# Kernel optimization log

Hardware: AMD Instinct MI355X
Metric: run time of the kernel (lower is better)

The kernel has to match this reference:

```python
import jax, jax.numpy as jnp
import numpy as np

H = 64          # nhid
L = 2           # nlayer
N_LEFT = 100000
N_RIGHT = 100000
E = 1000000
EPS = 1e-5

PNAMES = ["nn1_w1", "nn1_b1", "nn1_w2", "nn1_b2",
          "nn2_w1", "nn2_b1", "nn2_w2", "nn2_b2",
          "l1_w", "l1_b", "l2_w", "l2_b", "l3_w", "l3_b", "l4_w", "l4_b",
          "out_w1", "out_b1", "out_w2", "out_b2"]


def _bn_relu(x):
    # BatchNorm1d (training-mode batch stats, affine=False / default-init affine) + ReLU
    m = x.mean(0, keepdims=True)
    v = jnp.mean((x - m) ** 2, axis=0, keepdims=True)  # biased var, as torch BN
    return jax.nn.relu((x - m) * jax.lax.rsqrt(v + EPS))


def _mlp2(x, w1, b1, w2, b2):
    # MLP(nin, nout, nlayer=2, with_final_activation=True): (Linear->BN->ReLU) x2
    h = _bn_relu(x @ w1 + b1)
    return _bn_relu(h @ w2 + b2)


def _lin_bn_relu(x, w, b):
    # nn.Linear -> BatchNorm1d(affine=False) -> ReLU
    return _bn_relu(x @ w + b)


def _gscatter(msg, idx, n):
    # generalized_scatter with aggregators ['add','mean','max'], concatenated
    s = jax.ops.segment_sum(msg, idx, num_segments=n)
    cnt = jax.ops.segment_sum(jnp.ones((msg.shape[0],), msg.dtype), idx, num_segments=n)[:, None]
    mean = s / jnp.maximum(cnt, 1.0)
    mx = jax.ops.segment_max(msg, idx, num_segments=n)
    mx = jnp.where(cnt > 0, mx, 0.0)  # empty segments -> 0
    return jnp.concatenate([s, mean, mx], axis=-1)  # [n, 3*d]


def _parallel_layer(xs, src, dst, nl, p):
    # nl = n_left (static). combined_batch = [0]*nl + [1]*nr (sorted), last = 1.
    nr = xs.shape[0] - nl
    x_right = xs[nl:]                                   # batch != 0
    right_info = _gscatter(x_right[dst], src, nl)       # [nl, 3H]
    x_left_new = _mlp2(xs, p["nn1_w1"], p["nn1_b1"], p["nn1_w2"], p["nn1_b2"])[:nl]
    left_info = _gscatter(x_left_new[src], dst, nr)     # [nr, 3H]
    right_info_new = _mlp2(right_info, p["nn2_w1"], p["nn2_b1"], p["nn2_w2"], p["nn2_b2"])
    right_left_info = _gscatter(right_info_new[src], dst, nr)  # [nr, 3H]
    x = _lin_bn_relu(xs, p["l1_w"], p["l1_b"])                 # [N, H//2]
    ri = _lin_bn_relu(right_info, p["l2_w"], p["l2_b"])        # [nl, H//2]
    li = _lin_bn_relu(left_info, p["l3_w"], p["l3_b"])         # [nr, H//2]
    rli = _lin_bn_relu(right_left_info, p["l4_w"], p["l4_b"])  # [nr, H//2]
    # clone-and-masked-assign patterns become static-slice concatenations
    right_full = jnp.concatenate([ri, x[nl:]], axis=0)   # rows batch!=last <- ri
    left_full = jnp.concatenate([x[:nl], li], axis=0)    # rows batch!=0    <- li
    rl_full = jnp.concatenate([x[:nl], rli], axis=0)
    h = jnp.concatenate([x, right_full, left_full, rl_full], axis=-1)  # [N, 2H]
    return _mlp2(h, p["out_w1"], p["out_b1"], p["out_w2"], p["out_b2"])


def _forward(xs, params, src, dst, n_left):
    for l in range(L):
        p = {name: params[name][l] for name in PNAMES}
        xs = xs + _parallel_layer(xs, src, dst, n_left, p)  # residual; dropout=0, eval
    return xs  # output_encoder is Identity (nin == nout)


def setup_inputs() -> dict:
    key = jax.random.key(0)
    ks = iter(jax.random.split(key, 40))
    def w(shape, s=0.1):
        return jax.random.normal(next(ks), shape, jnp.float32) * s
    inp = {
        "xs": jax.random.normal(next(ks), (N_LEFT + N_RIGHT, H), jnp.float32),
        "nn1_w1": w((L, H, H)), "nn1_b1": w((L, H)),
        "nn1_w2": w((L, H, H)), "nn1_b2": w((L, H)),
        "nn2_w1": w((L, 3 * H, H)), "nn2_b1": w((L, H)),
        "nn2_w2": w((L, H, H)), "nn2_b2": w((L, H)),
        "l1_w": w((L, H, H // 2)), "l1_b": w((L, H // 2)),
        "l2_w": w((L, 3 * H, H // 2)), "l2_b": w((L, H // 2)),
        "l3_w": w((L, 3 * H, H // 2)), "l3_b": w((L, H // 2)),
        "l4_w": w((L, 3 * H, H // 2)), "l4_b": w((L, H // 2)),
        "out_w1": w((L, 2 * H, H)), "out_b1": w((L, H)),
        "out_w2": w((L, H, H)), "out_b2": w((L, H)),
        "src": jax.random.randint(next(ks), (E,), 0, N_LEFT),
        "dst": jax.random.randint(next(ks), (E,), 0, N_RIGHT),
        "n_left": N_LEFT,
    }
    return inp


def reference(xs, nn1_w1, nn1_b1, nn1_w2, nn1_b2, nn2_w1, nn2_b1, nn2_w2, nn2_b2,
              l1_w, l1_b, l2_w, l2_b, l3_w, l3_b, l4_w, l4_b,
              out_w1, out_b1, out_w2, out_b2, src, dst, n_left):
    params = dict(zip(PNAMES, (nn1_w1, nn1_b1, nn1_w2, nn1_b2,
                               nn2_w1, nn2_b1, nn2_w2, nn2_b2,
                               l1_w, l1_b, l2_w, l2_b, l3_w, l3_b, l4_w, l4_b,
                               out_w1, out_b1, out_w2, out_b2)))
    return _forward(xs, params, src, dst, int(n_left))
```

## Files before the change

kernel.cpp:

```cpp
#include <hip/hip_runtime.h>

#define NLEFT  100000
#define NRIGHT 100000
#define NTOT   200000
#define NEDGE  1000000
#define HD     64
#define BNEPS  1e-5f

typedef __attribute__((ext_vector_type(8))) short bfrag8;
typedef __attribute__((ext_vector_type(4))) float facc4;

__device__ inline unsigned short f2bf(float f) {
  unsigned u = __float_as_uint(f);
  u = u + 0x7fffu + ((u >> 16) & 1u);
  return (unsigned short)(u >> 16);
}
__device__ inline float bf2f(unsigned short u) {
  return __uint_as_float((unsigned)u << 16);
}

#define WC_G1    0
#define WC_G2    18432
#define WC_G3    24576
#define WC_NN2W2 30720
#define WC_M2    34816
#define WC_NN1W2 40960
#define WC_OUTW1 45056
#define WC_OUTW2 53248
#define WC_PER_L 57344


__global__ __launch_bounds__(256) void init_kernel(const float* __restrict__ xs,
                                                   float* __restrict__ out,
                                                   unsigned short* __restrict__ outbf,
                                                   float* __restrict__ st, int nst,
                                                   int* __restrict__ cl, int* __restrict__ cr,
                                                   int* __restrict__ curl, int* __restrict__ curr) {
  size_t ng = (size_t)NTOT * HD / 4;
  for (size_t i = (size_t)blockIdx.x * blockDim.x + threadIdx.x; i < ng;
       i += (size_t)gridDim.x * blockDim.x) {
    float4 v = reinterpret_cast<const float4*>(xs)[i];
    reinterpret_cast<float4*>(out)[i] = v;
    ushort4 p;
    p.x = f2bf(v.x); p.y = f2bf(v.y); p.z = f2bf(v.z); p.w = f2bf(v.w);
    reinterpret_cast<ushort4*>(outbf)[i] = p;
  }
  for (int i = blockIdx.x * blockDim.x + threadIdx.x; i < NLEFT;
       i += gridDim.x * blockDim.x) {
    cl[i] = 0; curl[i] = 0; cr[i] = 0; curr[i] = 0;
    if (i < nst) st[i] = 0.f;
  }
}

__global__ __launch_bounds__(256) void count_kernel(const int* __restrict__ src,
                                                    const int* __restrict__ dst,
                                                    int* __restrict__ cl, int* __restrict__ cr) {
  for (int e = blockIdx.x * blockDim.x + threadIdx.x; e < NEDGE;
       e += gridDim.x * blockDim.x) {
    atomicAdd(&cl[src[e]], 1);
    atomicAdd(&cr[dst[e]], 1);
  }
}


__global__ __launch_bounds__(256) void wconv_kernel(const float* __restrict__ l2w,
                                                    const float* __restrict__ nn2w1,
                                                    const float* __restrict__ l4w,
                                                    const float* __restrict__ l3w,
                                                    const float* __restrict__ nn2w2,
                                                    const float* __restrict__ nn1w1,
                                                    const float* __restrict__ l1w,
                                                    const float* __restrict__ nn1w2,
                                                    const float* __restrict__ outw1,
                                                    const float* __restrict__ outw2,
                                                    unsigned short* __restrict__ dst) {
  for (int idx = blockIdx.x * 256 + threadIdx.x; idx < 2 * WC_PER_L;
       idx += gridDim.x * 256) {
    int l = idx / WC_PER_L;
    int r = idx - l * WC_PER_L;
    const float* src; int N, n, k;
    if (r < WC_G2) {
      n = r / 192; k = r - n * 192;
      if (n < 32) { src = l2w + (size_t)l * 192 * 32; N = 32; }
      else        { src = nn2w1 + (size_t)l * 192 * 64; N = 64; n -= 32; }
    } else if (r < WC_G3) {
      int rr = r - WC_G2; n = rr / 192; k = rr - n * 192;
      src = l4w + (size_t)l * 192 * 32; N = 32;
    } else if (r < WC_NN2W2) {
      int rr = r - WC_G3; n = rr / 192; k = rr - n * 192;
      src = l3w + (size_t)l * 192 * 32; N = 32;
    } else if (r < WC_M2) {
      int rr = r - WC_NN2W2; n = rr / 64; k = rr - n * 64;
      src = nn2w2 + (size_t)l * 64 * 64; N = 64;
    } else if (r < WC_NN1W2) {
      int rr = r - WC_M2; n = rr / 64; k = rr - n * 64;
      if (n < 64) { src = nn1w1 + (size_t)l * 64 * 64; N = 64; }
      else        { src = l1w + (size_t)l * 64 * 32; N = 32; n -= 64; }
    } else if (r < WC_OUTW1) {
      int rr = r - WC_NN1W2; n = rr / 64; k = rr - n * 64;
      src = nn1w2 + (size_t)l * 64 * 64; N = 64;
    } else if (r < WC_OUTW2) {
      int rr = r - WC_OUTW1; n = rr / 128; k = rr - n * 128;
      src = outw1 + (size_t)l * 128 * 64; N = 64;
    } else {
      int rr = r - WC_OUTW2; n = rr / 64; k = rr - n * 64;
      src = outw2 + (size_t)l * 64 * 64; N = 64;
    }
    dst[idx] = f2bf(src[(size_t)k * N + n]);
  }
}


__global__ __launch_bounds__(256) void scan1_kernel(const int* __restrict__ cnt, int n,
                                                    int* __restrict__ partial) {
  __shared__ int tmp[256];
  int i = blockIdx.x * 256 + threadIdx.x;
  tmp[threadIdx.x] = (i < n) ? cnt[i] : 0;
  __syncthreads();
  for (int s = 128; s > 0; s >>= 1) {
    if (threadIdx.x < s) tmp[threadIdx.x] += tmp[threadIdx.x + s];
    __syncthreads();
  }
  if (threadIdx.x == 0) partial[blockIdx.x] = tmp[0];
}

__global__ __launch_bounds__(1024) void scan2_kernel(int* __restrict__ partial, int nb) {
  __shared__ int tmp[1024];
  int t = threadIdx.x;
  int v = (t < nb) ? partial[t] : 0;
  tmp[t] = v;
  __syncthreads();
  for (int off = 1; off < 1024; off <<= 1) {
    int x = tmp[t];
    int add = (t >= off) ? tmp[t - off] : 0;
    __syncthreads();
    tmp[t] = x + add;
    __syncthreads();
  }
  if (t < nb) partial[t] = tmp[t] - v;
}

__global__ __launch_bounds__(256) void scan3_kernel(const int* __restrict__ cnt, int n,
                                                    const int* __restrict__ partial,
                                                    int* __restrict__ offs) {
  __shared__ int tmp[256];
  int t = threadIdx.x;
  int i = blockIdx.x * 256 + t;
  int v = (i < n) ? cnt[i] : 0;
  tmp[t] = v;
  __syncthreads();
  for (int off = 1; off < 256; off <<= 1) {
    int x = tmp[t];
    int add = (t >= off) ? tmp[t - off] : 0;
    __syncthreads();
    tmp[t] = x + add;
    __syncthreads();
  }
  if (i < n) offs[i] = tmp[t] - v + partial[blockIdx.x];
  if (i == 0) offs[n] = NEDGE;
}


__global__ __launch_bounds__(256) void fill_kernel(const int* __restrict__ src,
                                                   const int* __restrict__ dst,
                                                   const int* __restrict__ oL,
                                                   const int* __restrict__ oR,
                                                   int* __restrict__ curL, int* __restrict__ curR,
                                                   int* __restrict__ adjL, int* __restrict__ adjR) {
  for (int e = blockIdx.x * blockDim.x + threadIdx.x; e < NEDGE;
       e += gridDim.x * blockDim.x) {
    int s = src[e], d = dst[e];
    int p = atomicAdd(&curL[s], 1);
    adjL[oL[s] + p] = d;
    int q = atomicAdd(&curR[d], 1);
    adjR[oR[d] + q] = s;
  }
}


template <int N1, int N2, bool SRCNORM>
__global__ __launch_bounds__(512) void gmm_mfma(const unsigned short* __restrict__ mat,
                                                const int* __restrict__ offs,
                                                const int* __restrict__ adj,
                                                int nseg,
                                                const float* __restrict__ st_src, float inv_src,
                                                const unsigned short* __restrict__ Wbf,
                                                const float* __restrict__ B1,
                                                unsigned short* __restrict__ Y1,
                                                float* __restrict__ st1,
                                                const float* __restrict__ B2,
                                                unsigned short* __restrict__ Y2,
                                                float* __restrict__ st2) {
  constexpr int K    = 192;
  constexpr int LDX  = 200;
  constexpr int SEGS = 32;
  constexpr int NT   = N1 + N2;
  constexpr int CTT  = NT / 16;
  constexpr int CTW  = (CTT >= 6) ? 2 : 1;
  constexpr int NGRP = CTT / CTW;
  constexpr int NWM  = 2 * NGRP;
  __shared__ alignas(16) unsigned short xl[SEGS * LDX];
  __shared__ alignas(16) unsigned short wl[NT * LDX];
  __shared__ float bl[NT];
  __shared__ float ldsS[NT], ldsQ[NT];

  int tid = threadIdx.x;
  for (int i = tid; i < NT * 24; i += 512) {
    int n = i / 24, kk = (i - n * 24) * 8;
    *reinterpret_cast<bfrag8*>(&wl[n * LDX + kk]) =
        *reinterpret_cast<const bfrag8*>(&Wbf[n * 192 + kk]);
  }
  for (int i = tid; i < N1; i += 512) bl[i] = B1[i];
  if constexpr (N2 > 0)
    for (int i = tid; i < N2; i += 512) bl[N1 + i] = B2[i];
  if (tid < NT) { ldsS[tid] = 0.f; ldsQ[tid] = 0.f; }

  int wave = tid >> 6;
  int lane = tid & 63;
  int half = lane >> 5;
  int c0   = (lane & 31) * 2;

  float nm0 = 0.f, nm1 = 0.f, ns0 = 1.f, ns1 = 1.f;
  if (SRCNORM) {
    float m0 = st_src[c0] * inv_src, m1 = st_src[c0 + 1] * inv_src;
    float v0 = st_src[64 + c0] * inv_src - m0 * m0;
    float v1 = st_src[64 + c0 + 1] * inv_src - m1 * m1;
    nm0 = m0; nm1 = m1;
    ns0 = rsqrtf(fmaxf(v0, 0.f) + BNEPS);
    ns1 = rsqrtf(fmaxf(v1, 0.f) + BNEPS);
  }

  int lr  = lane & 15;
  int lk  = (lane >> 4) * 8;
  int lj4 = (lane >> 4) * 4;
  int rowtile = wave & 1;
  int colgrp  = wave >> 1;
  int rowbase = rowtile * 16;

  float sacc[CTW], qacc[CTW];
#pragma unroll
  for (int ct = 0; ct < CTW; ct++) { sacc[ct] = 0.f; qacc[ct] = 0.f; }

  int tiles = (nseg + SEGS - 1) / SEGS;
  for (int t = blockIdx.x; t < tiles; t += gridDim.x) {
    __syncthreads();
    int segbase = t * SEGS + wave * 4;
    for (int s = 0; s < 4; s++) {
      int seg = segbase + s;
      int row = wave * 4 + s;
      float s0 = 0.f, s1 = 0.f, m0 = -INFINITY, m1 = -INFINITY;
      int cdeg = 0;
      if (seg < nseg) {
        int b = offs[seg], e = offs[seg + 1];
        cdeg = e - b;
        for (int jb = b + half; jb < e; jb += 16) {
          unsigned pk[8];
#pragma unroll
          for (int u = 0; u < 8; u++) {
            int j = jb + 2 * u;
            pk[u] = 0;
            if (j < e) {
              int g = adj[j];
              pk[u] = *reinterpret_cast<const unsigned*>(&mat[(size_t)g * HD + c0]);
            }
          }
#pragma unroll
          for (int u = 0; u < 8; u++) {
            int j = jb + 2 * u;
            if (j < e) {
              float v0 = __uint_as_float(pk[u] << 16);
              float v1 = __uint_as_float(pk[u] & 0xffff0000u);
              if (SRCNORM) {
                v0 = fmaxf((v0 - nm0) * ns0, 0.f);
                v1 = fmaxf((v1 - nm1) * ns1, 0.f);
              }
              s0 += v0; s1 += v1;
              m0 = fmaxf(m0, v0); m1 = fmaxf(m1, v1);
            }
          }
        }
        s0 += __shfl_xor(s0, 32);
        s1 += __shfl_xor(s1, 32);
        m0 = fmaxf(m0, __shfl_xor(m0, 32));
        m1 = fmaxf(m1, __shfl_xor(m1, 32));
      }
      float inv = 1.f / fmaxf((float)cdeg, 1.f);
      if (cdeg == 0) { m0 = 0.f; m1 = 0.f; s0 = 0.f; s1 = 0.f; }
      if (half == 0) {
        unsigned sp = (unsigned)f2bf(s0) | ((unsigned)f2bf(s1) << 16);
        unsigned mp = (unsigned)f2bf(m0) | ((unsigned)f2bf(m1) << 16);
        *reinterpret_cast<unsigned*>(&xl[row * LDX + c0])       = sp;
        *reinterpret_cast<unsigned*>(&xl[row * LDX + 128 + c0]) = mp;
      } else {
        unsigned ap = (unsigned)f2bf(s0 * inv) | ((unsigned)f2bf(s1 * inv) << 16);
        *reinterpret_cast<unsigned*>(&xl[row * LDX + 64 + c0]) = ap;
      }
    }
    __syncthreads();

    if (wave < NWM) {
      facc4 acc[CTW];
#pragma unroll
      for (int ct = 0; ct < CTW; ct++) acc[ct] = (facc4){0.f, 0.f, 0.f, 0.f};
#pragma unroll
      for (int kt = 0; kt < K / 32; kt++) {
        bfrag8 a = *reinterpret_cast<const bfrag8*>(&xl[(rowbase + lr) * LDX + kt * 32 + lk]);
#pragma unroll
        for (int ct = 0; ct < CTW; ct++) {
          bfrag8 b = *reinterpret_cast<const bfrag8*>(
              &wl[((colgrp * CTW + ct) * 16 + lr) * LDX + kt * 32 + lk]);
          acc[ct] = __builtin_amdgcn_mfma_f32_16x16x32_bf16(a, b, acc[ct], 0, 0, 0);
        }
      }
#pragma unroll
      for (int ct = 0; ct < CTW; ct++) {
        int col = (colgrp * CTW + ct) * 16 + lr;
        float bias = bl[col];
#pragma unroll
        for (int j = 0; j < 4; j++) {
          int grow = t * SEGS + rowbase + lj4 + j;
          if (grow < nseg) {
            float v = acc[ct][j] + bias;
            if (col < N1) Y1[(size_t)grow * N1 + col] = f2bf(v);
            else          Y2[(size_t)grow * N2 + (col - N1)] = f2bf(v);
            sacc[ct] += v; qacc[ct] += v * v;
          }
        }
      }
    }
  }

  __syncthreads();
  if (wave < NWM) {
#pragma unroll
    for (int ct = 0; ct < CTW; ct++) {
      int col = (colgrp * CTW + ct) * 16 + lr;
      atomicAdd(&ldsS[col], sacc[ct]);
      atomicAdd(&ldsQ[col], qacc[ct]);
    }
  }
  __syncthreads();
  if (tid < NT) {
    if (tid < N1) {
      atomicAdd(&st1[tid], ldsS[tid]);
      atomicAdd(&st1[N1 + tid], ldsQ[tid]);
    } else {
      atomicAdd(&st2[tid - N1], ldsS[tid]);
      atomicAdd(&st2[N2 + (tid - N1)], ldsQ[tid]);
    }
  }
}


__global__ __launch_bounds__(512) void gmm2_mfma(const unsigned short* __restrict__ matA,
                                                 const float* __restrict__ stA, float invA,
                                                 const unsigned short* __restrict__ matB,
                                                 const float* __restrict__ stB, float invB,
                                                 const int* __restrict__ offs,
                                                 const int* __restrict__ adj,
                                                 int nseg,
                                                 const unsigned short* __restrict__ Wbf,
                                                 const float* __restrict__ BA,
                                                 const float* __restrict__ BB,
                                                 unsigned short* __restrict__ YA,
                                                 float* __restrict__ st1,
                                                 unsigned short* __restrict__ YB,
                                                 float* __restrict__ st2) {
  constexpr int K = 192, LDX = 200, SEGS = 32;
  __shared__ alignas(16) unsigned short xlA[SEGS * LDX];
  __shared__ alignas(16) unsigned short xlB[SEGS * LDX];
  __shared__ alignas(16) unsigned short wl[64 * LDX];
  __shared__ float bl[64];
  __shared__ float ldsS[64], ldsQ[64];

  int tid = threadIdx.x;
  for (int i = tid; i < 64 * 24; i += 512) {
    int n = i / 24, kk = (i - n * 24) * 8;
    *reinterpret_cast<bfrag8*>(&wl[n * LDX + kk]) =
        *reinterpret_cast<const bfrag8*>(&Wbf[n * 192 + kk]);
  }
  if (tid < 32) bl[tid] = BA[tid];
  else if (tid < 64) bl[tid] = BB[tid - 32];
  if (tid < 64) { ldsS[tid] = 0.f; ldsQ[tid] = 0.f; }

  int wave = tid >> 6;
  int lane = tid & 63;
  int half = lane >> 5;
  int c0   = (lane & 31) * 2;

  float nmA0, nmA1, nsA0, nsA1, nmB0, nmB1, nsB0, nsB1;
  {
    float m0 = stA[c0] * invA, m1 = stA[c0 + 1] * invA;
    float v0 = stA[64 + c0] * invA - m0 * m0;
    float v1 = stA[64 + c0 + 1] * invA - m1 * m1;
    nmA0 = m0; nmA1 = m1;
    nsA0 = rsqrtf(fmaxf(v0, 0.f) + BNEPS);
    nsA1 = rsqrtf(fmaxf(v1, 0.f) + BNEPS);
    m0 = stB[c0] * invB; m1 = stB[c0 + 1] * invB;
    v0 = stB[64 + c0] * invB - m0 * m0;
    v1 = stB[64 + c0 + 1] * invB - m1 * m1;
    nmB0 = m0; nmB1 = m1;
    nsB0 = rsqrtf(fmaxf(v0, 0.f) + BNEPS);
    nsB1 = rsqrtf(fmaxf(v1, 0.f) + BNEPS);
  }

  int lr  = lane & 15;
  int lk  = (lane >> 4) * 8;
  int lj4 = (lane >> 4) * 4;
  int grp     = wave >> 2;
  int rowtile = wave & 1;
  int ctile   = (wave >> 1) & 1;
  int rowbase = rowtile * 16;

  float sacc = 0.f, qacc = 0.f;

  int tiles = (nseg + SEGS - 1) / SEGS;
  for (int t = blockIdx.x; t < tiles; t += gridDim.x) {
    __syncthreads();
    int segbase = t * SEGS + wave * 4;
    for (int s = 0; s < 4; s++) {
      int seg = segbase + s;
      int row = wave * 4 + s;
      float sA0 = 0.f, sA1 = 0.f, mA0 = -INFINITY, mA1 = -INFINITY;
      float sB0 = 0.f, sB1 = 0.f, mB0 = -INFINITY, mB1 = -INFINITY;
      int cdeg = 0;
      if (seg < nseg) {
        int b = offs[seg], e = offs[seg + 1];
        cdeg = e - b;
        for (int jb = b + half; jb < e; jb += 16) {
          unsigned pkA[8], pkB[8];
#pragma unroll
          for (int u = 0; u < 8; u++) {
            int j = jb + 2 * u;
            pkA[u] = 0; pkB[u] = 0;
            if (j < e) {
              int g = adj[j];
              pkA[u] = *reinterpret_cast<const unsigned*>(&matA[(size_t)g * HD + c0]);
              pkB[u] = *reinterpret_cast<const unsigned*>(&matB[(size_t)g * HD + c0]);
            }
          }
#pragma unroll
          for (int u = 0; u < 8; u++) {
            int j = jb + 2 * u;
            if (j < e) {
              float a0 = fmaxf((__uint_as_float(pkA[u] << 16) - nmA0) * nsA0, 0.f);
              float a1 = fmaxf((__uint_as_float(pkA[u] & 0xffff0000u) - nmA1) * nsA1, 0.f);
              float b0 = fmaxf((__uint_as_float(pkB[u] << 16) - nmB0) * nsB0, 0.f);
              float b1 = fmaxf((__uint_as_float(pkB[u] & 0xffff0000u) - nmB1) * nsB1, 0.f);
              sA0 += a0; sA1 += a1; mA0 = fmaxf(mA0, a0); mA1 = fmaxf(mA1, a1);
              sB0 += b0; sB1 += b1; mB0 = fmaxf(mB0, b0); mB1 = fmaxf(mB1, b1);
            }
          }
        }
        sA0 += __shfl_xor(sA0, 32);
        sA1 += __shfl_xor(sA1, 32);
        mA0 = fmaxf(mA0, __shfl_xor(mA0, 32));
        mA1 = fmaxf(mA1, __shfl_xor(mA1, 32));
        sB0 += __shfl_xor(sB0, 32);
        sB1 += __shfl_xor(sB1, 32);
        mB0 = fmaxf(mB0, __shfl_xor(mB0, 32));
        mB1 = fmaxf(mB1, __shfl_xor(mB1, 32));
      }
      float inv = 1.f / fmaxf((float)cdeg, 1.f);
      if (cdeg == 0) { mA0 = 0.f; mA1 = 0.f; mB0 = 0.f; mB1 = 0.f;
                       sA0 = 0.f; sA1 = 0.f; sB0 = 0.f; sB1 = 0.f; }
      if (half == 0) {
        *reinterpret_cast<unsigned*>(&xlA[row * LDX + c0]) =
            (unsigned)f2bf(sA0) | ((unsigned)f2bf(sA1) << 16);
        *reinterpret_cast<unsigned*>(&xlA[row * LDX + 128 + c0]) =
            (unsigned)f2bf(mA0) | ((unsigned)f2bf(mA1) << 16);
        *reinterpret_cast<unsigned*>(&xlB[row * LDX + c0]) =
            (unsigned)f2bf(sB0) | ((unsigned)f2bf(sB1) << 16);
        *reinterpret_cast<unsigned*>(&xlB[row * LDX + 128 + c0]) =
            (unsigned)f2bf(mB0) | ((unsigned)f2bf(mB1) << 16);
      } else {
        *reinterpret_cast<unsigned*>(&xlA[row * LDX + 64 + c0]) =
            (unsigned)f2bf(sA0 * inv) | ((unsigned)f2bf(sA1 * inv) << 16);
        *reinterpret_cast<unsigned*>(&xlB[row * LDX + 64 + c0]) =
            (unsigned)f2bf(sB0 * inv) | ((unsigned)f2bf(sB1 * inv) << 16);
      }
    }
    __syncthreads();

    {
      const unsigned short* xl = grp ? xlB : xlA;
      facc4 acc = (facc4){0.f, 0.f, 0.f, 0.f};
#pragma unroll
      for (int kt = 0; kt < K / 32; kt++) {
        bfrag8 a = *reinterpret_cast<const bfrag8*>(&xl[(rowbase + lr) * LDX + kt * 32 + lk]);
        bfrag8 b = *reinterpret_cast<const bfrag8*>(
            &wl[(grp * 32 + ctile * 16 + lr) * LDX + kt * 32 + lk]);
        acc = __builtin_amdgcn_mfma_f32_16x16x32_bf16(a, b, acc, 0, 0, 0);
      }
      int col = ctile * 16 + lr;
      float bias = bl[grp * 32 + col];
      unsigned short* Y = grp ? YB : YA;
#pragma unroll
      for (int j = 0; j < 4; j++) {
        int grow = t * SEGS + rowbase + lj4 + j;
        if (grow < nseg) {
          float v = acc[j] + bias;
          Y[(size_t)grow * 32 + col] = f2bf(v);
          sacc += v; qacc += v * v;
        }
      }
    }
  }

  __syncthreads();
  atomicAdd(&ldsS[grp * 32 + ctile * 16 + lr], sacc);
  atomicAdd(&ldsQ[grp * 32 + ctile * 16 + lr], qacc);
  __syncthreads();
  if (tid < 64) {
    if (tid < 32) {
      atomicAdd(&st1[tid], ldsS[tid]);
      atomicAdd(&st1[32 + tid], ldsQ[tid]);
    } else {
      atomicAdd(&st2[tid - 32], ldsS[tid]);
      atomicAdd(&st2[32 + (tid - 32)], ldsQ[tid]);
    }
  }
}


template <int K, int N, int ROWS, bool NIN>
__global__ __launch_bounds__(256) void mm_mfma(const unsigned short* __restrict__ X,
                                               const unsigned short* __restrict__ Wbf,
                                               const float* __restrict__ Bv,
                                               unsigned short* __restrict__ Y, int M,
                                               float* __restrict__ st_out,
                                               const float* __restrict__ st_in, float inv_m) {
  constexpr int LDX = K + 8;
  constexpr int RT  = ROWS / 64;
  constexpr int CT  = N / 16;
  constexpr int KV  = K / 8;
  __shared__ alignas(16) unsigned short xl[ROWS * LDX];
  __shared__ alignas(16) unsigned short wl[N * LDX];
  __shared__ float bl[N];
  __shared__ float nmean[K], nscal[K];
  __shared__ float ldsS[N], ldsQ[N];

  int tid = threadIdx.x;
  for (int i = tid; i < N * KV; i += 256) {
    int n = i / KV, kk = (i - n * KV) * 8;
    *reinterpret_cast<bfrag8*>(&wl[n * LDX + kk]) =
        *reinterpret_cast<const bfrag8*>(&Wbf[n * K + kk]);
  }
  for (int i = tid; i < N; i += 256) bl[i] = Bv[i];
  if (NIN) {
    for (int i = tid; i < K; i += 256) {
      float m = st_in[i] * inv_m;
      float v = st_in[K + i] * inv_m - m * m;
      nmean[i] = m;
      nscal[i] = rsqrtf(fmaxf(v, 0.f) + BNEPS);
    }
  }
  if (tid < N) { ldsS[tid] = 0.f; ldsQ[tid] = 0.f; }

  int lane = tid & 63;
  int wv   = tid >> 6;
  int lr   = lane & 15;
  int lk   = (lane >> 4) * 8;
  int lj4  = (lane >> 4) * 4;
  int rowbase = wv * (RT * 16);

  float sc[CT], sq[CT];
#pragma unroll
  for (int c = 0; c < CT; c++) { sc[c] = 0.f; sq[c] = 0.f; }

  int tiles = (M + ROWS - 1) / ROWS;
  for (int t = blockIdx.x; t < tiles; t += gridDim.x) {
    int r0 = t * ROWS;
    __syncthreads();
    for (int i = tid * 8; i < ROWS * K; i += 2048) {
      int r = i / K, c = i - r * K;
      int row = r0 + r;
      bfrag8 v = {0, 0, 0, 0, 0, 0, 0, 0};
      if (row < M) {
        v = *reinterpret_cast<const bfrag8*>(X + (size_t)row * K + c);
        if (NIN) {
#pragma unroll
          for (int j = 0; j < 8; j++) {
            float f = bf2f((unsigned short)v[j]);
            f = fmaxf((f - nmean[c + j]) * nscal[c + j], 0.f);
            v[j] = (short)f2bf(f);
          }
        }
      }
      *reinterpret_cast<bfrag8*>(&xl[r * LDX + c]) = v;
    }
    __syncthreads();

    facc4 acc[RT][CT];
#pragma unroll
    for (int rt = 0; rt < RT; rt++)
#pragma unroll
      for (int ct = 0; ct < CT; ct++) acc[rt][ct] = (facc4){0.f, 0.f, 0.f, 0.f};

#pragma unroll
    for (int kt = 0; kt < K / 32; kt++) {
      bfrag8 a[RT], b[CT];
#pragma unroll
      for (int rt = 0; rt < RT; rt++)
        a[rt] = *reinterpret_cast<const bfrag8*>(&xl[(rowbase + rt * 16 + lr) * LDX + kt * 32 + lk]);
#pragma unroll
      for (int ct = 0; ct < CT; ct++)
        b[ct] = *reinterpret_cast<const bfrag8*>(&wl[(ct * 16 + lr) * LDX + kt * 32 + lk]);
#pragma unroll
      for (int rt = 0; rt < RT; rt++)
#pragma unroll
        for (int ct = 0; ct < CT; ct++)
          acc[rt][ct] = __builtin_amdgcn_mfma_f32_16x16x32_bf16(a[rt], b[ct], acc[rt][ct], 0, 0, 0);
    }

#pragma unroll
    for (int rt = 0; rt < RT; rt++) {
#pragma unroll
      for (int ct = 0; ct < CT; ct++) {
        int col = ct * 16 + lr;
        float bcol = bl[col];
#pragma unroll
        for (int j = 0; j < 4; j++) {
          int row = r0 + rowbase + rt * 16 + lj4 + j;
          if (row < M) {
            float v = acc[rt][ct][j] + bcol;
            Y[(size_t)row * N + col] = f2bf(v);
            sc[ct] += v; sq[ct] += v * v;
          }
        }
      }
    }
  }

  __syncthreads();
#pragma unroll
  for (int ct = 0; ct < CT; ct++) {
    atomicAdd(&ldsS[ct * 16 + lr], sc[ct]);
    atomicAdd(&ldsQ[ct * 16 + lr], sq[ct]);
  }
  __syncthreads();
  if (tid < N) {
    atomicAdd(&st_out[tid], ldsS[tid]);
    atomicAdd(&st_out[N + tid], ldsQ[tid]);
  }
}


__global__ __launch_bounds__(256) void mm2_mfma(const unsigned short* __restrict__ X,
                                                const unsigned short* __restrict__ Wbf,
                                                const float* __restrict__ B1,
                                                unsigned short* __restrict__ Y1,
                                                float* __restrict__ st1,
                                                const float* __restrict__ B2,
                                                unsigned short* __restrict__ Y2,
                                                float* __restrict__ st2,
                                                int M) {
  constexpr int K = 64, N1 = 64, N2 = 32, NT = 96, ROWS = 128;
  constexpr int LDX = K + 8, RT = 2, CT = 6, KV = K / 8;
  __shared__ alignas(16) unsigned short xl[ROWS * LDX];
  __shared__ alignas(16) unsigned short wl[NT * LDX];
  __shared__ float bl[NT];
  __shared__ float ldsS[NT], ldsQ[NT];

  int tid = threadIdx.x;
  for (int i = tid; i < NT * KV; i += 256) {
    int n = i / KV, kk = (i - n * KV) * 8;
    *reinterpret_cast<bfrag8*>(&wl[n * LDX + kk]) =
        *reinterpret_cast<const bfrag8*>(&Wbf[n * K + kk]);
  }
  for (int i = tid; i < N1; i += 256) bl[i] = B1[i];
  for (int i = tid; i < N2; i += 256) bl[N1 + i] = B2[i];
  if (tid < NT) { ldsS[tid] = 0.f; ldsQ[tid] = 0.f; }

  int lane = tid & 63;
  int wv   = tid >> 6;
  int lr   = lane & 15;
  int lk   = (lane >> 4) * 8;
  int lj4  = (lane >> 4) * 4;
  int rowbase = wv * 32;

  float sc[CT], sq[CT];
#pragma unroll
  for (int c = 0; c < CT; c++) { sc[c] = 0.f; sq[c] = 0.f; }

  int tiles = (M + ROWS - 1) / ROWS;
  for (int t = blockIdx.x; t < tiles; t += gridDim.x) {
    int r0 = t * ROWS;
    __syncthreads();
    for (int i = tid * 8; i < ROWS * K; i += 2048) {
      int r = i / K, c = i - r * K;
      int row = r0 + r;
      bfrag8 v = {0, 0, 0, 0, 0, 0, 0, 0};
      if (row < M) v = *reinterpret_cast<const bfrag8*>(X + (size_t)row * K + c);
      *reinterpret_cast<bfrag8*>(&xl[r * LDX + c]) = v;
    }
    __syncthreads();

    facc4 acc[RT][CT];
#pragma unroll
    for (int rt = 0; rt < RT; rt++)
#pragma unroll
      for (int ct = 0; ct < CT; ct++) acc[rt][ct] = (facc4){0.f, 0.f, 0.f, 0.f};

#pragma unroll
    for (int kt = 0; kt < K / 32; kt++) {
      bfrag8 a[RT], b[CT];
#pragma unroll
      for (int rt = 0; rt < RT; rt++)
        a[rt] = *reinterpret_cast<const bfrag8*>(&xl[(rowbase + rt * 16 + lr) * LDX + kt * 32 + lk]);
#pragma unroll
      for (int ct = 0; ct < CT; ct++)
        b[ct] = *reinterpret_cast<const bfrag8*>(&wl[(ct * 16 + lr) * LDX + kt * 32 + lk]);
#pragma unroll
      for (int rt = 0; rt < RT; rt++)
#pragma unroll
        for (int ct = 0; ct < CT; ct++)
          acc[rt][ct] = __builtin_amdgcn_mfma_f32_16x16x32_bf16(a[rt], b[ct], acc[rt][ct], 0, 0, 0);
    }

#pragma unroll
    for (int rt = 0; rt < RT; rt++) {
#pragma unroll
      for (int ct = 0; ct < CT; ct++) {
        int col = ct * 16 + lr;
        float bcol = bl[col];
#pragma unroll
        for (int j = 0; j < 4; j++) {
          int row = r0 + rowbase + rt * 16 + lj4 + j;
          if (row < M) {
            float v = acc[rt][ct][j] + bcol;
            if (col < N1) Y1[(size_t)row * N1 + col] = f2bf(v);
            else          Y2[(size_t)row * N2 + (col - N1)] = f2bf(v);
            sc[ct] += v; sq[ct] += v * v;
          }
        }
      }
    }
  }

  __syncthreads();
#pragma unroll
  for (int ct = 0; ct < CT; ct++) {
    atomicAdd(&ldsS[ct * 16 + lr], sc[ct]);
    atomicAdd(&ldsQ[ct * 16 + lr], sq[ct]);
  }
  __syncthreads();
  if (tid < NT) {
    if (tid < N1) {
      atomicAdd(&st1[tid], ldsS[tid]);
      atomicAdd(&st1[N1 + tid], ldsQ[tid]);
    } else {
      atomicAdd(&st2[tid - N1], ldsS[tid]);
      atomicAdd(&st2[N2 + (tid - N1)], ldsQ[tid]);
    }
  }
}


__global__ __launch_bounds__(256) void mmh_mfma(const unsigned short* __restrict__ x32,
                                                const unsigned short* __restrict__ ri,
                                                const unsigned short* __restrict__ li,
                                                const unsigned short* __restrict__ rli,
                                                const float* __restrict__ stx,
                                                const float* __restrict__ stri,
                                                const float* __restrict__ stli,
                                                const float* __restrict__ strli,
                                                const unsigned short* __restrict__ Wbf,
                                                const float* __restrict__ Bv,
                                                unsigned short* __restrict__ Y,
                                                float* __restrict__ st_out) {
  constexpr int K = 128, N = 64, ROWS = 128, LDX = K + 8, RT = 2, CT = 4, KV = K / 8;
  __shared__ alignas(16) unsigned short xl[ROWS * LDX];
  __shared__ alignas(16) unsigned short wl[N * LDX];
  __shared__ float bl[N];
  __shared__ float m4[4 * 32], s4[4 * 32];
  __shared__ float ldsS[N], ldsQ[N];

  int tid = threadIdx.x;
  for (int i = tid; i < N * KV; i += 256) {
    int n = i / KV, kk = (i - n * KV) * 8;
    *reinterpret_cast<bfrag8*>(&wl[n * LDX + kk]) =
        *reinterpret_cast<const bfrag8*>(&Wbf[n * K + kk]);
  }
  for (int i = tid; i < N; i += 256) bl[i] = Bv[i];
  if (tid < 128) {
    int s = tid >> 5, c = tid & 31;
    const float* st = (s == 0) ? stx : (s == 1) ? stri : (s == 2) ? stli : strli;
    float inv = (s == 0) ? (1.f / NTOT) : (s == 1) ? (1.f / NLEFT) : (1.f / NRIGHT);
    float m = st[c] * inv;
    float v = st[32 + c] * inv - m * m;
    m4[tid] = m;
    s4[tid] = rsqrtf(fmaxf(v, 0.f) + BNEPS);
  }
  if (tid < N) { ldsS[tid] = 0.f; ldsQ[tid] = 0.f; }

  int lane = tid & 63;
  int wv   = tid >> 6;
  int lr   = lane & 15;
  int lk   = (lane >> 4) * 8;
  int lj4  = (lane >> 4) * 4;
  int rowbase = wv * 32;

  float sc[CT], sq[CT];
#pragma unroll
  for (int c = 0; c < CT; c++) { sc[c] = 0.f; sq[c] = 0.f; }

  const int M = NTOT;
  int tiles = (M + ROWS - 1) / ROWS;
  for (int t = blockIdx.x; t < tiles; t += gridDim.x) {
    int r0 = t * ROWS;
    __syncthreads();
    for (int i = tid * 8; i < ROWS * K; i += 2048) {
      int r = i / K, c = i - r * K;
      int row = r0 + r;
      bfrag8 v = {0, 0, 0, 0, 0, 0, 0, 0};
      if (row < M) {
        int cb = c >> 5, cc = c & 31;
        const unsigned short* srcp;
        int set, srow;
        if (row < NLEFT) {
          if (cb == 1) { srcp = ri;  set = 1; srow = row; }
          else         { srcp = x32; set = 0; srow = row; }
        } else {
          int rr = row - NLEFT;
          if (cb <= 1)      { srcp = x32; set = 0; srow = row; }
          else if (cb == 2) { srcp = li;  set = 2; srow = rr; }
          else              { srcp = rli; set = 3; srow = rr; }
        }
        v = *reinterpret_cast<const bfrag8*>(srcp + (size_t)srow * 32 + cc);
        const float* mm_ = &m4[set * 32 + cc];
        const float* ss_ = &s4[set * 32 + cc];
#pragma unroll
        for (int j = 0; j < 8; j++) {
          float f = bf2f((unsigned short)v[j]);
          f = fmaxf((f - mm_[j]) * ss_[j], 0.f);
          v[j] = (short)f2bf(f);
        }
      }
      *reinterpret_cast<bfrag8*>(&xl[r * LDX + c]) = v;
    }
    __syncthreads();

    facc4 acc[RT][CT];
#pragma unroll
    for (int rt = 0; rt < RT; rt++)
#pragma unroll
      for (int ct = 0; ct < CT; ct++) acc[rt][ct] = (facc4){0.f, 0.f, 0.f, 0.f};

#pragma unroll
    for (int kt = 0; kt < K / 32; kt++) {
      bfrag8 a[RT], b[CT];
#pragma unroll
      for (int rt = 0; rt < RT; rt++)
        a[rt] = *reinterpret_cast<const bfrag8*>(&xl[(rowbase + rt * 16 + lr) * LDX + kt * 32 + lk]);
#pragma unroll
      for (int ct = 0; ct < CT; ct++)
        b[ct] = *reinterpret_cast<const bfrag8*>(&wl[(ct * 16 + lr) * LDX + kt * 32 + lk]);
#pragma unroll
      for (int rt = 0; rt < RT; rt++)
#pragma unroll
        for (int ct = 0; ct < CT; ct++)
          acc[rt][ct] = __builtin_amdgcn_mfma_f32_16x16x32_bf16(a[rt], b[ct], acc[rt][ct], 0, 0, 0);
    }

#pragma unroll
    for (int rt = 0; rt < RT; rt++) {
#pragma unroll
      for (int ct = 0; ct < CT; ct++) {
        int col = ct * 16 + lr;
        float bcol = bl[col];
#pragma unroll
        for (int j = 0; j < 4; j++) {
          int row = r0 + rowbase + rt * 16 + lj4 + j;
          if (row < M) {
            float v = acc[rt][ct][j] + bcol;
            Y[(size_t)row * N + col] = f2bf(v);
            sc[ct] += v; sq[ct] += v * v;
          }
        }
      }
    }
  }

  __syncthreads();
#pragma unroll
  for (int ct = 0; ct < CT; ct++) {
    atomicAdd(&ldsS[ct * 16 + lr], sc[ct]);
    atomicAdd(&ldsQ[ct * 16 + lr], sq[ct]);
  }
  __syncthreads();
  if (tid < N) {
    atomicAdd(&st_out[tid], ldsS[tid]);
    atomicAdd(&st_out[N + tid], ldsQ[tid]);
  }
}


__global__ __launch_bounds__(256) void norm_add_kernel(const unsigned short* __restrict__ X, int M,
                                                       const float* __restrict__ st,
                                                       float* __restrict__ D,
                                                       unsigned short* __restrict__ Dbf) {
  __shared__ float mean[64], scal[64];
  if (threadIdx.x < 64) {
    float m = st[threadIdx.x] / (float)M;
    float v = st[64 + threadIdx.x] / (float)M - m * m;
    mean[threadIdx.x] = m;
    scal[threadIdx.x] = rsqrtf(fmaxf(v, 0.f) + BNEPS);
  }
  __syncthreads();
  size_t ngrp = (size_t)M * 64 / 8;
  for (size_t i = (size_t)blockIdx.x * 256 + threadIdx.x; i < ngrp;
       i += (size_t)gridDim.x * 256) {
    size_t base = i * 8;
    int c = (int)(base & 63);
    bfrag8 xv = *reinterpret_cast<const bfrag8*>(&X[base]);
    float4 d0 = *reinterpret_cast<float4*>(&D[base]);
    float4 d1 = *reinterpret_cast<float4*>(&D[base + 4]);
    float o[8];
#pragma unroll
    for (int j = 0; j < 8; j++) {
      float y = (bf2f((unsigned short)xv[j]) - mean[c + j]) * scal[c + j];
      y = y > 0.f ? y : 0.f;
      float dv = (j < 4) ? (&d0.x)[j] : (&d1.x)[j - 4];
      o[j] = dv + y;
    }
    d0 = make_float4(o[0], o[1], o[2], o[3]);
    d1 = make_float4(o[4], o[5], o[6], o[7]);
    *reinterpret_cast<float4*>(&D[base])     = d0;
    *reinterpret_cast<float4*>(&D[base + 4]) = d1;
    bfrag8 pb;
#pragma unroll
    for (int j = 0; j < 8; j++) pb[j] = (short)f2bf(o[j]);
    *reinterpret_cast<bfrag8*>(&Dbf[base]) = pb;
  }
}


static inline int tiles_of(int M, int R) { return (M + R - 1) / R; }
static inline int imin(int a, int b) { return a < b ? a : b; }

extern "C" void kernel_launch(void* const* d_in, const int* in_sizes, int n_in,
                              void* d_out, int out_size, void* d_ws, size_t ws_size,
                              hipStream_t stream) {
  const float* xs      = (const float*)d_in[0];
  const float* nn1_w1  = (const float*)d_in[1];
  const float* nn1_b1  = (const float*)d_in[2];
  const float* nn1_w2  = (const float*)d_in[3];
  const float* nn1_b2  = (const float*)d_in[4];
  const float* nn2_w1  = (const float*)d_in[5];
  const float* nn2_b1  = (const float*)d_in[6];
  const float* nn2_w2  = (const float*)d_in[7];
  const float* nn2_b2  = (const float*)d_in[8];
  const float* l1_w    = (const float*)d_in[9];
  const float* l1_b    = (const float*)d_in[10];
  const float* l2_w    = (const float*)d_in[11];
  const float* l2_b    = (const float*)d_in[12];
  const float* l3_w    = (const float*)d_in[13];
  const float* l3_b    = (const float*)d_in[14];
  const float* l4_w    = (const float*)d_in[15];
  const float* l4_b    = (const float*)d_in[16];
  const float* out_w1  = (const float*)d_in[17];
  const float* out_b1  = (const float*)d_in[18];
  const float* out_w2  = (const float*)d_in[19];
  const float* out_b2  = (const float*)d_in[20];
  const int*   src     = (const int*)d_in[21];
  const int*   dst     = (const int*)d_in[22];

  float* out = (float*)d_out;

  unsigned short* u     = (unsigned short*)d_ws;
  unsigned short* t1    = u;
  unsigned short* rin   = t1    + (size_t)NTOT * 64;
  unsigned short* x32   = rin   + (size_t)NLEFT * 64;
  unsigned short* ri32  = x32   + (size_t)NTOT * 32;
  unsigned short* li32  = ri32  + (size_t)NLEFT * 32;
  unsigned short* rli32 = li32  + (size_t)NRIGHT * 32;
  unsigned short* outbf = rli32 + (size_t)NRIGHT * 32;
  float* stats = (float*)(outbf + (size_t)NTOT * 64);
  int*   cntL  = (int*)(stats + 20 * 128);
  int*   cntR  = cntL + NLEFT;
  int*   oL    = cntR + NRIGHT;
  int*   oR    = oL + (NLEFT + 1);
  int*   curL  = oR + (NRIGHT + 1);
  int*   curR  = curL + NLEFT;
  int*   part  = curR + NRIGHT;
  int*   adjL  = part + 1024;
  int*   adjR  = adjL + NEDGE;
  unsigned short* wcvt = (unsigned short*)(adjR + NEDGE);

  dim3 B(256);
  const int NB1 = (NLEFT + 255) / 256;
  const float invL = 1.f / NLEFT, invT = 1.f / NTOT;
  const int tilesL = tiles_of(NLEFT, 32);
  const int GD = imin(tilesL, 768);

  init_kernel<<<2048, B, 0, stream>>>(xs, out, outbf, stats, 20 * 128, cntL, cntR, curL, curR);
  wconv_kernel<<<448, B, 0, stream>>>(l2_w, nn2_w1, l4_w, l3_w, nn2_w2, nn1_w1, l1_w,
                                      nn1_w2, out_w1, out_w2, wcvt);
  count_kernel<<<2048, B, 0, stream>>>(src, dst, cntL, cntR);
  scan1_kernel<<<NB1, B, 0, stream>>>(cntL, NLEFT, part);
  scan2_kernel<<<1, 1024, 0, stream>>>(part, NB1);
  scan3_kernel<<<NB1, B, 0, stream>>>(cntL, NLEFT, part, oL);
  scan1_kernel<<<NB1, B, 0, stream>>>(cntR, NRIGHT, part);
  scan2_kernel<<<1, 1024, 0, stream>>>(part, NB1);
  scan3_kernel<<<NB1, B, 0, stream>>>(cntR, NRIGHT, part, oR);
  fill_kernel<<<2048, B, 0, stream>>>(src, dst, oL, oR, curL, curR, adjL, adjR);

  for (int l = 0; l < 2; l++) {
    const float* p_nn1_b1 = nn1_b1 + (size_t)l * 64;
    const float* p_nn1_b2 = nn1_b2 + (size_t)l * 64;
    const float* p_nn2_b1 = nn2_b1 + (size_t)l * 64;
    const float* p_nn2_b2 = nn2_b2 + (size_t)l * 64;
    const float* p_l1_b   = l1_b + (size_t)l * 32;
    const float* p_l2_b   = l2_b + (size_t)l * 32;
    const float* p_l3_b   = l3_b + (size_t)l * 32;
    const float* p_l4_b   = l4_b + (size_t)l * 32;
    const float* p_out_b1 = out_b1 + (size_t)l * 64;
    const float* p_out_b2 = out_b2 + (size_t)l * 64;
    const unsigned short* wc = wcvt + (size_t)l * WC_PER_L;

    float* S = stats + (size_t)l * 10 * 128;
    auto ST = [&](int s) { return S + (size_t)s * 128; };

    gmm_mfma<32, 64, false><<<GD, 512, 0, stream>>>(
        outbf + (size_t)NLEFT * 64, oL, adjL, NLEFT, nullptr, 0.f,
        wc + WC_G1, p_l2_b, ri32, ST(0), p_nn2_b1, rin, ST(1));
    mm_mfma<64, 64, 128, true><<<tiles_of(NLEFT, 128), B, 0, stream>>>(
        rin, wc + WC_NN2W2, p_nn2_b2, rin, NLEFT, ST(2), ST(1), invL);
    mm2_mfma<<<tiles_of(NTOT, 128), B, 0, stream>>>(
        outbf, wc + WC_M2, p_nn1_b1, t1, ST(4), p_l1_b, x32, ST(7), NTOT);
    mm_mfma<64, 64, 128, true><<<tiles_of(NTOT, 128), B, 0, stream>>>(
        t1, wc + WC_NN1W2, p_nn1_b2, t1, NTOT, ST(5), ST(4), invT);
    gmm2_mfma<<<GD, 512, 0, stream>>>(
        rin, ST(2), invL, t1, ST(5), invT, oR, adjR, NRIGHT,
        wc + WC_G2, p_l4_b, p_l3_b, rli32, ST(3), li32, ST(6));
    mmh_mfma<<<tiles_of(NTOT, 128), B, 0, stream>>>(
        x32, ri32, li32, rli32, ST(7), ST(0), ST(6), ST(3),
        wc + WC_OUTW1, p_out_b1, t1, ST(8));
    mm_mfma<64, 64, 128, true><<<tiles_of(NTOT, 128), B, 0, stream>>>(
        t1, wc + WC_OUTW2, p_out_b2, t1, NTOT, ST(9), ST(8), invT);
    norm_add_kernel<<<2048, B, 0, stream>>>(t1, NTOT, ST(9), out, outbf);
  }
}
```

Before: 1.148 ms.

## Build CSR adjacency via two-pass bucketed binning instead of random atomic fill

Replaces the single-pass CSR fill with three steps. A prefix pass computes per-bucket offsets over 512-node buckets. Each edge is then binned into its bucket as an (owner, neighbor) pair. Finally, one block per bucket scatters its edges into the adjacency arrays. The goal is to confine the per-node atomics and adjacency writes to a small, cache-resident address range per block instead of hitting random locations across the whole graph. In exchange it adds an extra pass, extra staging memory, and heavy atomic contention on only 196 bucket counters during binning.

```diff
diff --git a/kernel.cpp b/kernel.cpp
--- a/kernel.cpp
+++ b/kernel.cpp
@@ -6,6 +6,8 @@
 #define NEDGE  1000000
 #define HD     64
 #define BNEPS  1e-5f
+#define BSH    9
+#define NBKT   196
 
 typedef __attribute__((ext_vector_type(8))) short bfrag8;
 typedef __attribute__((ext_vector_type(4))) float facc4;
@@ -161,19 +163,58 @@
 }
 
 
-__global__ __launch_bounds__(256) void fill_kernel(const int* __restrict__ src,
-                                                   const int* __restrict__ dst,
-                                                   const int* __restrict__ oL,
-                                                   const int* __restrict__ oR,
-                                                   int* __restrict__ curL, int* __restrict__ curR,
-                                                   int* __restrict__ adjL, int* __restrict__ adjR) {
+__global__ __launch_bounds__(256) void bucket_kernel(const int* __restrict__ cntL,
+                                                     const int* __restrict__ cntR,
+                                                     int* __restrict__ bcurL,
+                                                     int* __restrict__ bcurR) {
+  __shared__ int bl[NBKT], br[NBKT];
+  int t = threadIdx.x;
+  if (t < NBKT) {
+    int sL = 0, sR = 0;
+    int k0 = t << BSH;
+    int k1 = k0 + (1 << BSH); if (k1 > NLEFT) k1 = NLEFT;
+    for (int k = k0; k < k1; k++) { sL += cntL[k]; sR += cntR[k]; }
+    bl[t] = sL; br[t] = sR;
+  }
+  __syncthreads();
+  if (t == 0) {
+    int aL = 0, aR = 0;
+    for (int b = 0; b < NBKT; b++) {
+      int cl = bl[b], cr = br[b];
+      bcurL[b] = aL; bcurR[b] = aR;
+      aL += cl; aR += cr;
+    }
+  }
+}
+
+__global__ __launch_bounds__(256) void bin_kernel(const int* __restrict__ src,
+                                                  const int* __restrict__ dst,
+                                                  int* __restrict__ bcurL,
+                                                  int* __restrict__ bcurR,
+                                                  int2* __restrict__ binL,
+                                                  int2* __restrict__ binR) {
   for (int e = blockIdx.x * blockDim.x + threadIdx.x; e < NEDGE;
        e += gridDim.x * blockDim.x) {
     int s = src[e], d = dst[e];
-    int p = atomicAdd(&curL[s], 1);
-    adjL[oL[s] + p] = d;
-    int q = atomicAdd(&curR[d], 1);
-    adjR[oR[d] + q] = s;
+    int pL = atomicAdd(&bcurL[s >> BSH], 1);
+    binL[pL] = make_int2(s, d);
+    int pR = atomicAdd(&bcurR[d >> BSH], 1);
+    binR[pR] = make_int2(d, s);
+  }
+}
+
+__global__ __launch_bounds__(256) void scatter_kernel(const int2* __restrict__ bin,
+                                                      const int* __restrict__ bcur,
+                                                      const int* __restrict__ offs,
+                                                      int* __restrict__ cur,
+                                                      int* __restrict__ adj) {
+  int b = blockIdx.x;
+  int lo = (b == 0) ? 0 : bcur[b - 1];
+  int hi = bcur[b];
+  for (int i = lo + threadIdx.x; i < hi; i += 256) {
+    int2 p = bin[i];
+    int pos = atomicAdd(&cur[p.x], 1);
+    adj[offs[p.x] + pos] = p.y;
   }
 }
 
@@ -987,6 +1028,10 @@
   int*   adjL  = part + 1024;
   int*   adjR  = adjL + NEDGE;
   unsigned short* wcvt = (unsigned short*)(adjR + NEDGE);
+  int2*  binL  = (int2*)(wcvt + 2 * WC_PER_L);
+  int2*  binR  = binL + NEDGE;
+  int*   bcurL = (int*)(binR + NEDGE);
+  int*   bcurR = bcurL + 256;
 
   dim3 B(256);
   const int NB1 = (NLEFT + 255) / 256;
@@ -1004,7 +1049,10 @@
   scan1_kernel<<<NB1, B, 0, stream>>>(cntR, NRIGHT, part);
   scan2_kernel<<<1, 1024, 0, stream>>>(part, NB1);
   scan3_kernel<<<NB1, B, 0, stream>>>(cntR, NRIGHT, part, oR);
-  fill_kernel<<<2048, B, 0, stream>>>(src, dst, oL, oR, curL, curR, adjL, adjR);
+  bucket_kernel<<<1, B, 0, stream>>>(cntL, cntR, bcurL, bcurR);
+  bin_kernel<<<2048, B, 0, stream>>>(src, dst, bcurL, bcurR, binL, binR);
+  scatter_kernel<<<NBKT, B, 0, stream>>>(binL, bcurL, oL, curL, adjL);
+  scatter_kernel<<<NBKT, B, 0, stream>>>(binR, bcurR, oR, curR, adjR);
 
   for (int l = 0; l < 2; l++) {
     const float* p_nn1_b1 = nn1_b1 + (size_t)l * 64;
```

After: 1.849 ms. +61.1%, slower.
